# Performance work log

Measured on AMD Instinct MI355X. Metric: run time of the kernel, lower is better.

## Reference

```python
import jax, jax.numpy as jnp
import numpy as np

B, L, D = 16, 2048, 320          # batch, frames, mel_filter_size * mask_size (80*4)
CODE_DIM = 16                     # code_book_size (projection output dim)
NUM_CODES = 8192                  # num_code_books (codebook entries)
N_MASK = (B * L) // 2             # fixed number of masked positions (static for jit)


def setup_inputs() -> dict:
    key = jax.random.key(0)
    k1, k2, k3, k4 = jax.random.split(key, 4)
    input_values = jax.random.normal(k1, (B, L, D), dtype=jnp.float32)
    # mask with exactly N_MASK ones so the gather has a static size
    perm = jax.random.permutation(k2, B * L)
    mask_flat = jnp.zeros((B * L,), jnp.int32).at[perm[:N_MASK]].set(1)
    mask_time_indices = mask_flat.reshape(B, L)
    # xavier_uniform for Linear(D -> CODE_DIM), weight shape (CODE_DIM, D)
    limit = float(np.sqrt(6.0 / (D + CODE_DIM)))
    proj_weight = jax.random.uniform(k3, (CODE_DIM, D), jnp.float32, -limit, limit)
    code_book = jax.random.normal(k4, (NUM_CODES, CODE_DIM), dtype=jnp.float32)
    return {
        "input_values": input_values,
        "mask_time_indices": mask_time_indices,
        "proj_weight": proj_weight,
        "code_book": code_book,
    }


def reference(input_values, mask_time_indices, proj_weight, code_book):
    d = input_values.shape[-1]
    x = input_values.reshape(-1, d)                      # (B*L, D)
    mask = mask_time_indices.reshape(-1)
    idx = jnp.nonzero(mask == 1, size=N_MASK)[0]         # static-size gather of masked rows
    rows = x[idx]                                        # (N, D)
    targets = rows @ proj_weight.T                       # (N, CODE_DIM)
    # ||t - c||_2 via the GEMM expansion ||t||^2 + ||c||^2 - 2 t.c (avoids (N,K,S) blowup)
    t2 = jnp.sum(targets * targets, axis=-1, keepdims=True)       # (N, 1)
    c2 = jnp.sum(code_book * code_book, axis=-1)                  # (K,)
    d2 = t2 + c2[None, :] - 2.0 * (targets @ code_book.T)         # (N, K)
    dist = jnp.sqrt(jnp.maximum(d2, 0.0))
    # torch.argmin with no dim flattens -> scalar index into the (N*K) array
    labels = jnp.argmin(dist)
    return labels
```

## Files before the change

### kernel.cpp

```cpp
#include <hip/hip_runtime.h>
#include <hip/hip_bf16.h>


#define NMASK   16384
#define NROWS   32768
#define D       320
#define CDIM    16
#define NCODES  8192
#define EPS_C   0.0117f
#define EPS_ABS 0.02f

typedef __attribute__((ext_vector_type(8))) short short8;
typedef __attribute__((ext_vector_type(4))) float f32x4;

__device__ inline unsigned int encf(float f) {
  unsigned int u = __float_as_uint(f);
  return (u & 0x80000000u) ? ~u : (u | 0x80000000u);
}
__device__ inline float decf(unsigned int u) {
  unsigned int b = (u & 0x80000000u) ? (u & 0x7fffffffu) : ~u;
  return __uint_as_float(b);
}
__device__ inline unsigned short f2bf(float f) {
  unsigned int u = __float_as_uint(f);
  unsigned int r = u + 0x7fffu + ((u >> 16) & 1u);
  return (unsigned short)(r >> 16);
}
__device__ inline float bf2f(unsigned short h) {
  return __uint_as_float(((unsigned int)h) << 16);
}

__device__ inline void proj_lds(const float* __restrict__ x,
                                const float* __restrict__ Wl,
                                int row, int ch, float pd[16]) {
  const float* xr = x + (size_t)row * D + ch * 4;
  float4 xv[10];
#pragma unroll
  for (int j = 0; j < 10; ++j) xv[j] = *(const float4*)(xr + j * 32);
#pragma unroll
  for (int c = 0; c < 16; ++c) pd[c] = 0.f;
#pragma unroll
  for (int j = 0; j < 10; ++j) {
#pragma unroll
    for (int c = 0; c < 16; ++c) {
      const float4 wv = *(const float4*)&Wl[c * D + j * 32 + ch * 4];
      float acc = fmaf(xv[j].x, wv.x, pd[c]);
      acc = fmaf(xv[j].y, wv.y, acc);
      acc = fmaf(xv[j].z, wv.z, acc);
      pd[c] = fmaf(xv[j].w, wv.w, acc);
    }
  }
#pragma unroll
  for (int c = 0; c < 16; ++c) {
    pd[c] += __shfl_xor(pd[c], 1);
    pd[c] += __shfl_xor(pd[c], 2);
    pd[c] += __shfl_xor(pd[c], 4);
  }
}

__global__ void init_kernel(unsigned int* __restrict__ ctrs,
                            unsigned long long* __restrict__ key) {
  if (threadIdx.x < 4) ctrs[threadIdx.x] = 0u;
  if (threadIdx.x == 4) key[0] = 0xFFFFFFFFFFFFFFFFull;
}

__global__ __launch_bounds__(256) void project_kernel(
    const float* __restrict__ x, const int* __restrict__ mask,
    const float* __restrict__ W, const float* __restrict__ cbk,
    float* __restrict__ c2, unsigned short* __restrict__ cbf32,
    unsigned short* __restrict__ tbf32, float* __restrict__ t2arr,
    int* __restrict__ origrow, unsigned int* __restrict__ rowmin_u,
    unsigned int* __restrict__ slotctr) {
  __shared__ float Wl[CDIM * D];
  __shared__ unsigned long long mb;
  __shared__ unsigned int wcnt[4], wbase[4];
  int tid = threadIdx.x, bid = (int)blockIdx.x;
  int chunk = bid >> 1, half = bid & 1;
  for (int i = tid; i < (CDIM * D) / 4; i += 256)
    ((float4*)Wl)[i] = ((const float4*)W)[i];
  if (tid < 64) {
    int m = mask[chunk * 64 + tid];
    unsigned long long bal = __ballot(m != 0);
    if (tid == 0) mb = bal;
  }
  if (tid < 16) rowmin_u[bid * 16 + tid] = 0xFFFFFFFFu;
  __syncthreads();

  if (bid < 512 && tid < 16) {
    int k = bid * 16 + tid;
    const float4* p = (const float4*)(cbk + (long)k * CDIM);
    float s = 0.f; unsigned short nb[16];
#pragma unroll
    for (int q = 0; q < 4; ++q) {
      float4 v = p[q];
      s = fmaf(v.x, v.x, s); s = fmaf(v.y, v.y, s);
      s = fmaf(v.z, v.z, s); s = fmaf(v.w, v.w, s);
      nb[q*4+0] = f2bf(-2.0f * v.x); nb[q*4+1] = f2bf(-2.0f * v.y);
      nb[q*4+2] = f2bf(-2.0f * v.z); nb[q*4+3] = f2bf(-2.0f * v.w);
    }
    c2[k] = s;
    unsigned short g1 = f2bf(s);
    unsigned short g2 = f2bf(s - bf2f(g1));
    uint4 pk0, pk1, pk2, pk3;
    pk0.x = (unsigned int)nb[0]  | ((unsigned int)nb[1]  << 16);
    pk0.y = (unsigned int)nb[2]  | ((unsigned int)nb[3]  << 16);
    pk0.z = (unsigned int)nb[4]  | ((unsigned int)nb[5]  << 16);
    pk0.w = (unsigned int)nb[6]  | ((unsigned int)nb[7]  << 16);
    pk1.x = (unsigned int)nb[8]  | ((unsigned int)nb[9]  << 16);
    pk1.y = (unsigned int)nb[10] | ((unsigned int)nb[11] << 16);
    pk1.z = (unsigned int)nb[12] | ((unsigned int)nb[13] << 16);
    pk1.w = (unsigned int)nb[14] | ((unsigned int)nb[15] << 16);
    pk2.x = (unsigned int)g1 | ((unsigned int)g2 << 16);
    pk2.y = 0x3F803F80u;
    pk2.z = 0u; pk2.w = 0u;
    pk3.x = 0u; pk3.y = 0u; pk3.z = 0u; pk3.w = 0u;
    uint4* dst = (uint4*)(cbf32 + (long)k * 32);
    dst[0] = pk0; dst[1] = pk1; dst[2] = pk2; dst[3] = pk3;
  }

  unsigned long long B0 = mb;
  int r = tid >> 3, ch = tid & 7, lane = tid & 63, w = tid >> 6;
  int p = half * 32 + r;
  int row = chunk * 64 + p;
  int m = (int)((B0 >> p) & 1ull);

  unsigned long long wbal = __ballot(m && ch == 0);
  if (lane == 0) wcnt[w] = (unsigned int)__popcll(wbal);
  __syncthreads();
  if (tid == 0) {
    unsigned int tot = wcnt[0] + wcnt[1] + wcnt[2] + wcnt[3];
    unsigned int b = tot ? atomicAdd(slotctr, tot) : 0u;
    wbase[0] = b;
    wbase[1] = b + wcnt[0];
    wbase[2] = b + wcnt[0] + wcnt[1];
    wbase[3] = b + wcnt[0] + wcnt[1] + wcnt[2];
  }
  __syncthreads();
  if (!m) return;

  float pd[16];
  proj_lds(x, Wl, row, ch, pd);

  if (ch == 0) {
    int slot = (int)wbase[w] + __popcll(wbal & ((1ull << lane) - 1ull));
    float t2 = 0.f;
#pragma unroll
    for (int c = 0; c < 16; ++c) t2 = fmaf(pd[c], pd[c], t2);
    t2arr[slot] = t2;
    origrow[slot] = row;
    unsigned short tb[16];
#pragma unroll
    for (int c = 0; c < 16; ++c) tb[c] = f2bf(pd[c]);
    unsigned short h1 = f2bf(t2);
    unsigned short h2 = f2bf(t2 - bf2f(h1));
    uint4 pk0, pk1, pk2, pk3;
    pk0.x = (unsigned int)tb[0]  | ((unsigned int)tb[1]  << 16);
    pk0.y = (unsigned int)tb[2]  | ((unsigned int)tb[3]  << 16);
    pk0.z = (unsigned int)tb[4]  | ((unsigned int)tb[5]  << 16);
    pk0.w = (unsigned int)tb[6]  | ((unsigned int)tb[7]  << 16);
    pk1.x = (unsigned int)tb[8]  | ((unsigned int)tb[9]  << 16);
    pk1.y = (unsigned int)tb[10] | ((unsigned int)tb[11] << 16);
    pk1.z = (unsigned int)tb[12] | ((unsigned int)tb[13] << 16);
    pk1.w = (unsigned int)tb[14] | ((unsigned int)tb[15] << 16);
    pk2.x = 0x3F803F80u;
    pk2.y = (unsigned int)h1 | ((unsigned int)h2 << 16);
    pk2.z = 0u; pk2.w = 0u;
    pk3.x = 0u; pk3.y = 0u; pk3.z = 0u; pk3.w = 0u;
    uint4* dst = (uint4*)(tbf32 + (long)slot * 32);
    dst[0] = pk0; dst[1] = pk1; dst[2] = pk2; dst[3] = pk3;
  }
}

__global__ __launch_bounds__(256) void phase1_kernel(
    const unsigned short* __restrict__ tbf32,
    const unsigned short* __restrict__ cbf32,
    unsigned int* __restrict__ rowmin_u) {
  __shared__ unsigned int rml[4 * 33];
  int tid = threadIdx.x;
  int w = tid >> 6, l = tid & 63, lr = l & 15, g = l >> 4;
  int strip = (int)blockIdx.x >> 2;
  int seg   = ((int)blockIdx.x & 3) * 4 + w;
  int row0 = strip * 32;

  for (int i = tid; i < 4 * 33; i += 256) rml[i] = 0xFFFFFFFFu;
  __syncthreads();

  const f32x4 zero = {0.f, 0.f, 0.f, 0.f};
  short8 calA = {0,0,0,0,0,0,0,0}, calB = {0,0,0,0,0,0,0,0};
  if (g == 0) {
    calA[0] = (short)f2bf((float)(lr + 1));
    calB[0] = (short)0x3F80;
  }
  f32x4 cal = __builtin_amdgcn_mfma_f32_16x16x32_bf16(calA, calB, zero, 0, 0, 0);
  int rid[4];
#pragma unroll
  for (int j = 0; j < 4; ++j) {
    int v = (int)(cal[j] + 0.5f) - 1;
    rid[j] = v < 0 ? 0 : (v > 15 ? 15 : v);
  }

  const short8 a0 = *(const short8*)(tbf32 + (long)(row0 + lr) * 32 + g * 8);
  const short8 a1 = *(const short8*)(tbf32 + (long)(row0 + 16 + lr) * 32 + g * 8);
  f32x4 rmin0 = {3.4e38f, 3.4e38f, 3.4e38f, 3.4e38f};
  f32x4 rmin1 = rmin0;
  int code0 = seg * 512;
#pragma unroll 2
  for (int t = 0; t < 32; ++t) {
    int code = code0 + t * 16 + lr;
    short8 b = *(const short8*)(cbf32 + (long)code * 32 + g * 8);
    f32x4 d0 = __builtin_amdgcn_mfma_f32_16x16x32_bf16(a0, b, zero, 0, 0, 0);
    f32x4 d1 = __builtin_amdgcn_mfma_f32_16x16x32_bf16(a1, b, zero, 0, 0, 0);
#pragma unroll
    for (int j = 0; j < 4; ++j) {
      rmin0[j] = fminf(rmin0[j], d0[j]);
      rmin1[j] = fminf(rmin1[j], d1[j]);
    }
  }
  unsigned int* mywave = &rml[w * 33];
#pragma unroll
  for (int j = 0; j < 4; ++j) {
    atomicMin(&mywave[rid[j]],      encf(rmin0[j]));
    atomicMin(&mywave[16 + rid[j]], encf(rmin1[j]));
  }
  __syncthreads();
  if (tid < 32) {
    unsigned int mn = 0xFFFFFFFFu;
#pragma unroll
    for (int ww = 0; ww < 4; ++ww) mn = min(mn, rml[ww * 33 + tid]);
    atomicMin(&rowmin_u[row0 + tid], mn);
  }
}

__global__ __launch_bounds__(1024) void gate_kernel(
    const unsigned int* __restrict__ rowmin_u, const float* __restrict__ t2arr,
    const float* __restrict__ c2,
    unsigned int* __restrict__ candcount, int* __restrict__ candlist) {
  __shared__ float sT[1024];
  __shared__ float c2m_s;
  __shared__ unsigned int cnt;
  int tid = threadIdx.x;
  float cm = 0.f;
#pragma unroll
  for (int i = 0; i < 8; ++i) cm = fmaxf(cm, c2[tid + i * 1024]);
  sT[tid] = cm;
  if (tid == 0) cnt = 0u;
  __syncthreads();
  for (int st = 512; st > 0; st >>= 1) {
    if (tid < st) sT[tid] = fmaxf(sT[tid], sT[tid + st]);
    __syncthreads();
  }
  if (tid == 0) c2m_s = sT[0];
  __syncthreads();
  float c2m = c2m_s;
  float Tl = 3.4e38f;
  for (int i = tid; i < NMASK; i += 1024) {
    float a = decf(rowmin_u[i]);
    float e = fmaf(EPS_C, sqrtf(t2arr[i] * c2m), EPS_ABS);
    Tl = fminf(Tl, a + e);
  }
  sT[tid] = Tl;
  __syncthreads();
  for (int st = 512; st > 0; st >>= 1) {
    if (tid < st) sT[tid] = fminf(sT[tid], sT[tid + st]);
    __syncthreads();
  }
  float T = sT[0];
  for (int i = tid; i < NMASK; i += 1024) {
    float a = decf(rowmin_u[i]);
    float e = fmaf(EPS_C, sqrtf(t2arr[i] * c2m), EPS_ABS);
    if (!(a - e > T)) {
      unsigned int pos = atomicAdd(&cnt, 1u);
      candlist[pos] = i;
    }
  }
  __syncthreads();
  if (tid == 0) candcount[0] = cnt;
}

__global__ __launch_bounds__(256) void cproj_kernel(
    const float* __restrict__ x, const float* __restrict__ W,
    const int* __restrict__ origrow, const unsigned int* __restrict__ candcount,
    const int* __restrict__ candlist, float* __restrict__ tgtm) {
  int tid = threadIdx.x, bid = (int)blockIdx.x;
  int nc = (int)candcount[0];
  if (bid * 32 >= nc) return;
  __shared__ float Wl[CDIM * D];
  for (int i = tid; i < (CDIM * D) / 4; i += 256)
    ((float4*)Wl)[i] = ((const float4*)W)[i];
  __syncthreads();
  int idx = bid * 32 + (tid >> 3);
  int ch  = tid & 7;
  if (idx >= nc) return;
  int row = origrow[candlist[idx]];
  float pd[16];
  proj_lds(x, Wl, row, ch, pd);
  if (ch == 0) {
    float* op = tgtm + (long)idx * 16;
#pragma unroll
    for (int c = 0; c < 16; ++c) op[c] = -2.0f * pd[c];
  }
}

__global__ __launch_bounds__(256) void rescore_kernel(
    const float* __restrict__ cbk, const float* __restrict__ c2,
    const float* __restrict__ tgtm, const float* __restrict__ t2arr,
    const int* __restrict__ origrow, const int* __restrict__ mask,
    const unsigned int* __restrict__ candcount, const int* __restrict__ candlist,
    unsigned long long* __restrict__ key, unsigned int* __restrict__ resctr,
    int* __restrict__ out) {
  __shared__ unsigned long long red[256];
  __shared__ int lastf;
  __shared__ unsigned int vlow_s;
  int tid = threadIdx.x, bid = (int)blockIdx.x;
  int nwork = (int)candcount[0] * 8;
  for (int wk = bid; wk < nwork; wk += (int)gridDim.x) {
    int ci = wk >> 3, oct = wk & 7;
    int r = candlist[ci];
    float t2 = t2arr[r];
    int row = origrow[r];
    float tm[16];
    const float4* tp = (const float4*)(tgtm + (long)ci * 16);
#pragma unroll
    for (int q = 0; q < 4; ++q) {
      float4 v = tp[q];
      tm[q*4+0] = v.x; tm[q*4+1] = v.y; tm[q*4+2] = v.z; tm[q*4+3] = v.w;
    }
    float minv = 3.4e38f; int mink = 0;
#pragma unroll 2
    for (int k = 0; k < 4; ++k) {
      int code = oct * 1024 + k * 256 + tid;
      const float4* cp = (const float4*)(cbk + (long)code * CDIM);
      float4 c0 = cp[0], c1 = cp[1], c2v4 = cp[2], c3 = cp[3];
      float acc = fmaf(tm[0],  c0.x, c2[code]);
      acc = fmaf(tm[1],  c0.y, acc);   acc = fmaf(tm[2],  c0.z, acc);
      acc = fmaf(tm[3],  c0.w, acc);   acc = fmaf(tm[4],  c1.x, acc);
      acc = fmaf(tm[5],  c1.y, acc);   acc = fmaf(tm[6],  c1.z, acc);
      acc = fmaf(tm[7],  c1.w, acc);   acc = fmaf(tm[8],  c2v4.x, acc);
      acc = fmaf(tm[9],  c2v4.y, acc); acc = fmaf(tm[10], c2v4.z, acc);
      acc = fmaf(tm[11], c2v4.w, acc); acc = fmaf(tm[12], c3.x, acc);
      acc = fmaf(tm[13], c3.y, acc);   acc = fmaf(tm[14], c3.z, acc);
      acc = fmaf(tm[15], c3.w, acc);
      if (acc < minv) { minv = acc; mink = code; }
    }
    red[tid] = ((unsigned long long)encf(t2 + minv) << 32)
        | (unsigned long long)((unsigned int)row * (unsigned int)NCODES + (unsigned int)mink);
    __syncthreads();
    for (int s = 128; s > 0; s >>= 1) {
      if (tid < s) { if (red[tid + s] < red[tid]) red[tid] = red[tid + s]; }
      __syncthreads();
    }
    if (tid == 0) atomicMin(key, red[0]);
    __syncthreads();
  }
  if (tid == 0) {
    __threadfence();
    lastf = (atomicAdd(resctr, 1u) == (unsigned int)gridDim.x - 1u) ? 1 : 0;
  }
  __syncthreads();
  if (lastf) {
    if (tid == 0)
      vlow_s = (unsigned int)(atomicMin(key, 0xFFFFFFFFFFFFFFFFull) & 0xFFFFFFFFull);
    __syncthreads();
    unsigned int vlow = vlow_s;
    int wrow = (int)(vlow >> 13), wcode = (int)(vlow & 8191u);
    int lo = tid * (NROWS / 256);
    int hi = lo + (NROWS / 256); if (hi > wrow) hi = wrow;
    int cnt = 0;
#pragma unroll 4
    for (int i = lo; i < hi; ++i) cnt += (mask[i] != 0);
    __shared__ int ps[256];
    ps[tid] = cnt;
    __syncthreads();
    for (int s = 128; s > 0; s >>= 1) {
      if (tid < s) ps[tid] += ps[tid + s];
      __syncthreads();
    }
    if (tid == 0) out[0] = ps[0] * NCODES + wcode;
  }
}

extern "C" void kernel_launch(void* const* d_in, const int* in_sizes, int n_in,
                              void* d_out, int out_size, void* d_ws, size_t ws_size,
                              hipStream_t stream) {
  const float* x    = (const float*)d_in[0];
  const int*   mask = (const int*)d_in[1];
  const float* W    = (const float*)d_in[2];
  const float* cbk  = (const float*)d_in[3];
  int* out = (int*)d_out;

  char* ws = (char*)d_ws;
  unsigned int*       ctrs      = (unsigned int*)(ws + 4096);
  unsigned int*       resctr    = (unsigned int*)(ws + 4096);
  unsigned int*       slotctr   = (unsigned int*)(ws + 4100);
  unsigned int*       candcount = (unsigned int*)(ws + 4112);
  unsigned long long* key       = (unsigned long long*)(ws + 8184);
  unsigned int*       rowmin_u  = (unsigned int*)(ws + 8192);
  float*              t2arr     = (float*)(ws + 73728);
  int*                origrow   = (int*)(ws + 139264);
  float*              c2        = (float*)(ws + 204800);
  unsigned short*     cbf32     = (unsigned short*)(ws + 237568);
  int*                candlist  = (int*)(ws + 237568);
  unsigned short*     tbf32     = (unsigned short*)(ws + 761856);
  float*              tgtm      = (float*)(ws + 761856);

  init_kernel<<<1, 64, 0, stream>>>(ctrs, key);
  project_kernel<<<1024, 256, 0, stream>>>(x, mask, W, cbk, c2, cbf32, tbf32,
                                           t2arr, origrow, rowmin_u, slotctr);
  phase1_kernel<<<2048, 256, 0, stream>>>(tbf32, cbf32, rowmin_u);
  gate_kernel<<<1, 1024, 0, stream>>>(rowmin_u, t2arr, c2, candcount, candlist);
  cproj_kernel<<<512, 256, 0, stream>>>(x, W, origrow, candcount, candlist, tgtm);
  rescore_kernel<<<512, 256, 0, stream>>>(cbk, c2, tgtm, t2arr, origrow, mask,
                                          candcount, candlist, key, resctr, out);
}
```

Before: 89.37 us.

## Fuse gate, candidate projection and rescore into one single-block tail kernel

Merges the gate, candidate projection and rescore kernels into one 1024-thread single-block tail kernel, removing two launches, the global key atomics and the last-block counter. Phase1 now has each block cover all 8192 codes for its 32-row strip (512 blocks instead of 2048). Row minima can then be stored directly instead of reduced with atomicMin, so the rowmin init is dropped. The cost is that the whole rescore over candidates runs serially in one block, which becomes slow if many candidates pass the gate.

After: 124.6 us. +39.4%, slower.

```diff
diff --git a/kernel.cpp b/kernel.cpp
--- a/kernel.cpp
+++ b/kernel.cpp
@@ -58,10 +58,8 @@
   }
 }
 
-__global__ void init_kernel(unsigned int* __restrict__ ctrs,
-                            unsigned long long* __restrict__ key) {
+__global__ void init_kernel(unsigned int* __restrict__ ctrs) {
   if (threadIdx.x < 4) ctrs[threadIdx.x] = 0u;
-  if (threadIdx.x == 4) key[0] = 0xFFFFFFFFFFFFFFFFull;
 }
 
 __global__ __launch_bounds__(256) void project_kernel(
@@ -69,8 +67,7 @@
     const float* __restrict__ W, const float* __restrict__ cbk,
     float* __restrict__ c2, unsigned short* __restrict__ cbf32,
     unsigned short* __restrict__ tbf32, float* __restrict__ t2arr,
-    int* __restrict__ origrow, unsigned int* __restrict__ rowmin_u,
-    unsigned int* __restrict__ slotctr) {
+    int* __restrict__ origrow, unsigned int* __restrict__ slotctr) {
   __shared__ float Wl[CDIM * D];
   __shared__ unsigned long long mb;
   __shared__ unsigned int wcnt[4], wbase[4];
@@ -83,7 +80,6 @@
     unsigned long long bal = __ballot(m != 0);
     if (tid == 0) mb = bal;
   }
-  if (tid < 16) rowmin_u[bid * 16 + tid] = 0xFFFFFFFFu;
   __syncthreads();
 
   if (bid < 512 && tid < 16) {
@@ -178,12 +174,9 @@
   __shared__ unsigned int rml[4 * 33];
   int tid = threadIdx.x;
   int w = tid >> 6, l = tid & 63, lr = l & 15, g = l >> 4;
-  int strip = (int)blockIdx.x >> 2;
-  int seg   = ((int)blockIdx.x & 3) * 4 + w;
-  int row0 = strip * 32;
+  int row0 = (int)blockIdx.x * 32;
 
   for (int i = tid; i < 4 * 33; i += 256) rml[i] = 0xFFFFFFFFu;
-  __syncthreads();
 
   const f32x4 zero = {0.f, 0.f, 0.f, 0.f};
   short8 calA = {0,0,0,0,0,0,0,0}, calB = {0,0,0,0,0,0,0,0};
@@ -203,19 +196,23 @@
   const short8 a1 = *(const short8*)(tbf32 + (long)(row0 + 16 + lr) * 32 + g * 8);
   f32x4 rmin0 = {3.4e38f, 3.4e38f, 3.4e38f, 3.4e38f};
   f32x4 rmin1 = rmin0;
-  int code0 = seg * 512;
+#pragma unroll
+  for (int s4 = 0; s4 < 4; ++s4) {
+    int code0 = (s4 * 4 + w) * 512;
 #pragma unroll 2
-  for (int t = 0; t < 32; ++t) {
-    int code = code0 + t * 16 + lr;
-    short8 b = *(const short8*)(cbf32 + (long)code * 32 + g * 8);
-    f32x4 d0 = __builtin_amdgcn_mfma_f32_16x16x32_bf16(a0, b, zero, 0, 0, 0);
-    f32x4 d1 = __builtin_amdgcn_mfma_f32_16x16x32_bf16(a1, b, zero, 0, 0, 0);
-#pragma unroll
-    for (int j = 0; j < 4; ++j) {
-      rmin0[j] = fminf(rmin0[j], d0[j]);
-      rmin1[j] = fminf(rmin1[j], d1[j]);
-    }
-  }
+    for (int t = 0; t < 32; ++t) {
+      int code = code0 + t * 16 + lr;
+      short8 b = *(const short8*)(cbf32 + (long)code * 32 + g * 8);
+      f32x4 d0 = __builtin_amdgcn_mfma_f32_16x16x32_bf16(a0, b, zero, 0, 0, 0);
+      f32x4 d1 = __builtin_amdgcn_mfma_f32_16x16x32_bf16(a1, b, zero, 0, 0, 0);
+#pragma unroll
+      for (int j = 0; j < 4; ++j) {
+        rmin0[j] = fminf(rmin0[j], d0[j]);
+        rmin1[j] = fminf(rmin1[j], d1[j]);
+      }
+    }
+  }
+  __syncthreads();
   unsigned int* mywave = &rml[w * 33];
 #pragma unroll
   for (int j = 0; j < 4; ++j) {
@@ -227,97 +224,77 @@
     unsigned int mn = 0xFFFFFFFFu;
 #pragma unroll
     for (int ww = 0; ww < 4; ++ww) mn = min(mn, rml[ww * 33 + tid]);
-    atomicMin(&rowmin_u[row0 + tid], mn);
-  }
-}
-
-__global__ __launch_bounds__(1024) void gate_kernel(
-    const unsigned int* __restrict__ rowmin_u, const float* __restrict__ t2arr,
-    const float* __restrict__ c2,
-    unsigned int* __restrict__ candcount, int* __restrict__ candlist) {
-  __shared__ float sT[1024];
-  __shared__ float c2m_s;
-  __shared__ unsigned int cnt;
+    rowmin_u[row0 + tid] = mn;
+  }
+}
+
+__global__ __launch_bounds__(1024) void tail_kernel(
+    const float* __restrict__ x, const float* __restrict__ W,
+    const float* __restrict__ cbk, const float* __restrict__ c2,
+    const float* __restrict__ t2arr, const int* __restrict__ origrow,
+    const unsigned int* __restrict__ rowmin_u, const int* __restrict__ mask,
+    int* __restrict__ candlist, float* __restrict__ tgtm,
+    int* __restrict__ out) {
+  __shared__ float Wl[CDIM * D];
+  __shared__ float red_f[1024];
+  __shared__ unsigned long long red_u[1024];
+  __shared__ unsigned int cnt_s;
+  __shared__ unsigned int vlow_s;
   int tid = threadIdx.x;
+
+  for (int i = tid; i < (CDIM * D) / 4; i += 1024)
+    ((float4*)Wl)[i] = ((const float4*)W)[i];
   float cm = 0.f;
-#pragma unroll
-  for (int i = 0; i < 8; ++i) cm = fmaxf(cm, c2[tid + i * 1024]);
-  sT[tid] = cm;
-  if (tid == 0) cnt = 0u;
-  __syncthreads();
-  for (int st = 512; st > 0; st >>= 1) {
-    if (tid < st) sT[tid] = fmaxf(sT[tid], sT[tid + st]);
+  for (int i = tid; i < NCODES; i += 1024) cm = fmaxf(cm, c2[i]);
+  red_f[tid] = cm;
+  if (tid == 0) cnt_s = 0u;
+  __syncthreads();
+  for (int s = 512; s > 0; s >>= 1) {
+    if (tid < s) red_f[tid] = fmaxf(red_f[tid], red_f[tid + s]);
     __syncthreads();
   }
-  if (tid == 0) c2m_s = sT[0];
-  __syncthreads();
-  float c2m = c2m_s;
+  float c2m = red_f[0];
+  __syncthreads();
   float Tl = 3.4e38f;
   for (int i = tid; i < NMASK; i += 1024) {
     float a = decf(rowmin_u[i]);
     float e = fmaf(EPS_C, sqrtf(t2arr[i] * c2m), EPS_ABS);
     Tl = fminf(Tl, a + e);
   }
-  sT[tid] = Tl;
-  __syncthreads();
-  for (int st = 512; st > 0; st >>= 1) {
-    if (tid < st) sT[tid] = fminf(sT[tid], sT[tid + st]);
+  red_f[tid] = Tl;
+  __syncthreads();
+  for (int s = 512; s > 0; s >>= 1) {
+    if (tid < s) red_f[tid] = fminf(red_f[tid], red_f[tid + s]);
     __syncthreads();
   }
-  float T = sT[0];
+  float T = red_f[0];
   for (int i = tid; i < NMASK; i += 1024) {
     float a = decf(rowmin_u[i]);
     float e = fmaf(EPS_C, sqrtf(t2arr[i] * c2m), EPS_ABS);
     if (!(a - e > T)) {
-      unsigned int pos = atomicAdd(&cnt, 1u);
+      unsigned int pos = atomicAdd(&cnt_s, 1u);
       candlist[pos] = i;
     }
   }
   __syncthreads();
-  if (tid == 0) candcount[0] = cnt;
-}
-
-__global__ __launch_bounds__(256) void cproj_kernel(
-    const float* __restrict__ x, const float* __restrict__ W,
-    const int* __restrict__ origrow, const unsigned int* __restrict__ candcount,
-    const int* __restrict__ candlist, float* __restrict__ tgtm) {
-  int tid = threadIdx.x, bid = (int)blockIdx.x;
-  int nc = (int)candcount[0];
-  if (bid * 32 >= nc) return;
-  __shared__ float Wl[CDIM * D];
-  for (int i = tid; i < (CDIM * D) / 4; i += 256)
-    ((float4*)Wl)[i] = ((const float4*)W)[i];
-  __syncthreads();
-  int idx = bid * 32 + (tid >> 3);
-  int ch  = tid & 7;
-  if (idx >= nc) return;
-  int row = origrow[candlist[idx]];
-  float pd[16];
-  proj_lds(x, Wl, row, ch, pd);
-  if (ch == 0) {
-    float* op = tgtm + (long)idx * 16;
-#pragma unroll
-    for (int c = 0; c < 16; ++c) op[c] = -2.0f * pd[c];
-  }
-}
-
-__global__ __launch_bounds__(256) void rescore_kernel(
-    const float* __restrict__ cbk, const float* __restrict__ c2,
-    const float* __restrict__ tgtm, const float* __restrict__ t2arr,
-    const int* __restrict__ origrow, const int* __restrict__ mask,
-    const unsigned int* __restrict__ candcount, const int* __restrict__ candlist,
-    unsigned long long* __restrict__ key, unsigned int* __restrict__ resctr,
-    int* __restrict__ out) {
-  __shared__ unsigned long long red[256];
-  __shared__ int lastf;
-  __shared__ unsigned int vlow_s;
-  int tid = threadIdx.x, bid = (int)blockIdx.x;
-  int nwork = (int)candcount[0] * 8;
-  for (int wk = bid; wk < nwork; wk += (int)gridDim.x) {
-    int ci = wk >> 3, oct = wk & 7;
-    int r = candlist[ci];
-    float t2 = t2arr[r];
-    int row = origrow[r];
+  int nc = (int)cnt_s;
+  int grp = tid >> 3, ch = tid & 7;
+  for (int idx = grp; idx < nc; idx += 128) {
+    int row = origrow[candlist[idx]];
+    float pd[16];
+    proj_lds(x, Wl, row, ch, pd);
+    if (ch == 0) {
+      float* op = tgtm + (long)idx * 16;
+#pragma unroll
+      for (int c = 0; c < 16; ++c) op[c] = -2.0f * pd[c];
+    }
+  }
+  __syncthreads();
+  unsigned long long best = 0xFFFFFFFFFFFFFFFFull;
+  for (int ci = 0; ci < nc; ++ci) {
+    int slot = candlist[ci];
+    float t2 = t2arr[slot];
+    int row = origrow[slot];
     float tm[16];
     const float4* tp = (const float4*)(tgtm + (long)ci * 16);
 #pragma unroll
@@ -325,10 +302,9 @@
       float4 v = tp[q];
       tm[q*4+0] = v.x; tm[q*4+1] = v.y; tm[q*4+2] = v.z; tm[q*4+3] = v.w;
     }
-    float minv = 3.4e38f; int mink = 0;
 #pragma unroll 2
-    for (int k = 0; k < 4; ++k) {
-      int code = oct * 1024 + k * 256 + tid;
+    for (int k = 0; k < 8; ++k) {
+      int code = k * 1024 + tid;
       const float4* cp = (const float4*)(cbk + (long)code * CDIM);
       float4 c0 = cp[0], c1 = cp[1], c2v4 = cp[2], c3 = cp[3];
       float acc = fmaf(tm[0],  c0.x, c2[code]);
@@ -340,43 +316,34 @@
       acc = fmaf(tm[11], c2v4.w, acc); acc = fmaf(tm[12], c3.x, acc);
       acc = fmaf(tm[13], c3.y, acc);   acc = fmaf(tm[14], c3.z, acc);
       acc = fmaf(tm[15], c3.w, acc);
-      if (acc < minv) { minv = acc; mink = code; }
-    }
-    red[tid] = ((unsigned long long)encf(t2 + minv) << 32)
-        | (unsigned long long)((unsigned int)row * (unsigned int)NCODES + (unsigned int)mink);
+      unsigned long long pk = ((unsigned long long)encf(t2 + acc) << 32)
+          | (unsigned long long)((unsigned int)row * (unsigned int)NCODES
+                                 + (unsigned int)code);
+      best = (pk < best) ? pk : best;
+    }
+  }
+  red_u[tid] = best;
+  __syncthreads();
+  for (int s = 512; s > 0; s >>= 1) {
+    if (tid < s) { if (red_u[tid + s] < red_u[tid]) red_u[tid] = red_u[tid + s]; }
     __syncthreads();
-    for (int s = 128; s > 0; s >>= 1) {
-      if (tid < s) { if (red[tid + s] < red[tid]) red[tid] = red[tid + s]; }
-      __syncthreads();
-    }
-    if (tid == 0) atomicMin(key, red[0]);
+  }
+  if (tid == 0) vlow_s = (unsigned int)(red_u[0] & 0xFFFFFFFFull);
+  __syncthreads();
+  unsigned int vlow = vlow_s;
+  int wrow = (int)(vlow >> 13), wcode = (int)(vlow & 8191u);
+  int lo = tid * (NROWS / 1024);
+  int hi = lo + (NROWS / 1024); if (hi > wrow) hi = wrow;
+  int cnt = 0;
+#pragma unroll 4
+  for (int i = lo; i < hi; ++i) cnt += (mask[i] != 0);
+  red_u[tid] = (unsigned long long)cnt;
+  __syncthreads();
+  for (int s = 512; s > 0; s >>= 1) {
+    if (tid < s) red_u[tid] += red_u[tid + s];
     __syncthreads();
   }
-  if (tid == 0) {
-    __threadfence();
-    lastf = (atomicAdd(resctr, 1u) == (unsigned int)gridDim.x - 1u) ? 1 : 0;
-  }
-  __syncthreads();
-  if (lastf) {
-    if (tid == 0)
-      vlow_s = (unsigned int)(atomicMin(key, 0xFFFFFFFFFFFFFFFFull) & 0xFFFFFFFFull);
-    __syncthreads();
-    unsigned int vlow = vlow_s;
-    int wrow = (int)(vlow >> 13), wcode = (int)(vlow & 8191u);
-    int lo = tid * (NROWS / 256);
-    int hi = lo + (NROWS / 256); if (hi > wrow) hi = wrow;
-    int cnt = 0;
-#pragma unroll 4
-    for (int i = lo; i < hi; ++i) cnt += (mask[i] != 0);
-    __shared__ int ps[256];
-    ps[tid] = cnt;
-    __syncthreads();
-    for (int s = 128; s > 0; s >>= 1) {
-      if (tid < s) ps[tid] += ps[tid + s];
-      __syncthreads();
-    }
-    if (tid == 0) out[0] = ps[0] * NCODES + wcode;
-  }
+  if (tid == 0) out[0] = (int)red_u[0] * NCODES + wcode;
 }
 
 extern "C" void kernel_launch(void* const* d_in, const int* in_sizes, int n_in,
@@ -390,10 +357,7 @@
 
   char* ws = (char*)d_ws;
   unsigned int*       ctrs      = (unsigned int*)(ws + 4096);
-  unsigned int*       resctr    = (unsigned int*)(ws + 4096);
-  unsigned int*       slotctr   = (unsigned int*)(ws + 4100);
-  unsigned int*       candcount = (unsigned int*)(ws + 4112);
-  unsigned long long* key       = (unsigned long long*)(ws + 8184);
+  unsigned int*       slotctr   = (unsigned int*)(ws + 4096);
   unsigned int*       rowmin_u  = (unsigned int*)(ws + 8192);
   float*              t2arr     = (float*)(ws + 73728);
   int*                origrow   = (int*)(ws + 139264);
@@ -403,12 +367,10 @@
   unsigned short*     tbf32     = (unsigned short*)(ws + 761856);
   float*              tgtm      = (float*)(ws + 761856);
 
-  init_kernel<<<1, 64, 0, stream>>>(ctrs, key);
+  init_kernel<<<1, 64, 0, stream>>>(ctrs);
   project_kernel<<<1024, 256, 0, stream>>>(x, mask, W, cbk, c2, cbf32, tbf32,
-                                           t2arr, origrow, rowmin_u, slotctr);
-  phase1_kernel<<<2048, 256, 0, stream>>>(tbf32, cbf32, rowmin_u);
-  gate_kernel<<<1, 1024, 0, stream>>>(rowmin_u, t2arr, c2, candcount, candlist);
-  cproj_kernel<<<512, 256, 0, stream>>>(x, W, origrow, candcount, candlist, tgtm);
-  rescore_kernel<<<512, 256, 0, stream>>>(cbk, c2, tgtm, t2arr, origrow, mask,
-                                          candcount, candlist, key, resctr, out);
-}
+                                           t2arr, origrow, slotctr);
+  phase1_kernel<<<512, 256, 0, stream>>>(tbf32, cbf32, rowmin_u);
+  tail_kernel<<<1, 1024, 0, stream>>>(x, W, cbk, c2, t2arr, origrow, rowmin_u,
+                                      mask, candlist, tgtm, out);
+}
```

## Make phase1 own full codebook per strip and fuse gate with candidate projection

Applied to the files above, without the earlier changes.

Each phase1 block now loops over all 16 codebook segments for its 32-row strip, so it writes row minima directly instead of doing global atomicMin, and project_kernel no longer has to initialize rowmin_u. The gate kernel and candidate projection kernel are merged into one single-block kernel, which removes a launch and the candcount readback. In exchange, phase1 launches 4x fewer blocks with 4x longer loops, and candidate projection now runs on only one workgroup, so it is serialized if many candidates pass the gate.

Result: slower. 115.7 us (+29.5%).

```diff
diff --git a/kernel.cpp b/kernel.cpp
--- a/kernel.cpp
+++ b/kernel.cpp
@@ -69,8 +69,7 @@
     const float* __restrict__ W, const float* __restrict__ cbk,
     float* __restrict__ c2, unsigned short* __restrict__ cbf32,
     unsigned short* __restrict__ tbf32, float* __restrict__ t2arr,
-    int* __restrict__ origrow, unsigned int* __restrict__ rowmin_u,
-    unsigned int* __restrict__ slotctr) {
+    int* __restrict__ origrow, unsigned int* __restrict__ slotctr) {
   __shared__ float Wl[CDIM * D];
   __shared__ unsigned long long mb;
   __shared__ unsigned int wcnt[4], wbase[4];
@@ -83,7 +82,6 @@
     unsigned long long bal = __ballot(m != 0);
     if (tid == 0) mb = bal;
   }
-  if (tid < 16) rowmin_u[bid * 16 + tid] = 0xFFFFFFFFu;
   __syncthreads();
 
   if (bid < 512 && tid < 16) {
@@ -178,12 +176,9 @@
   __shared__ unsigned int rml[4 * 33];
   int tid = threadIdx.x;
   int w = tid >> 6, l = tid & 63, lr = l & 15, g = l >> 4;
-  int strip = (int)blockIdx.x >> 2;
-  int seg   = ((int)blockIdx.x & 3) * 4 + w;
-  int row0 = strip * 32;
+  int row0 = (int)blockIdx.x * 32;
 
   for (int i = tid; i < 4 * 33; i += 256) rml[i] = 0xFFFFFFFFu;
-  __syncthreads();
 
   const f32x4 zero = {0.f, 0.f, 0.f, 0.f};
   short8 calA = {0,0,0,0,0,0,0,0}, calB = {0,0,0,0,0,0,0,0};
@@ -203,19 +198,23 @@
   const short8 a1 = *(const short8*)(tbf32 + (long)(row0 + 16 + lr) * 32 + g * 8);
   f32x4 rmin0 = {3.4e38f, 3.4e38f, 3.4e38f, 3.4e38f};
   f32x4 rmin1 = rmin0;
-  int code0 = seg * 512;
+#pragma unroll
+  for (int s4 = 0; s4 < 4; ++s4) {
+    int code0 = (s4 * 4 + w) * 512;
 #pragma unroll 2
-  for (int t = 0; t < 32; ++t) {
-    int code = code0 + t * 16 + lr;
-    short8 b = *(const short8*)(cbf32 + (long)code * 32 + g * 8);
-    f32x4 d0 = __builtin_amdgcn_mfma_f32_16x16x32_bf16(a0, b, zero, 0, 0, 0);
-    f32x4 d1 = __builtin_amdgcn_mfma_f32_16x16x32_bf16(a1, b, zero, 0, 0, 0);
-#pragma unroll
-    for (int j = 0; j < 4; ++j) {
-      rmin0[j] = fminf(rmin0[j], d0[j]);
-      rmin1[j] = fminf(rmin1[j], d1[j]);
-    }
-  }
+    for (int t = 0; t < 32; ++t) {
+      int code = code0 + t * 16 + lr;
+      short8 b = *(const short8*)(cbf32 + (long)code * 32 + g * 8);
+      f32x4 d0 = __builtin_amdgcn_mfma_f32_16x16x32_bf16(a0, b, zero, 0, 0, 0);
+      f32x4 d1 = __builtin_amdgcn_mfma_f32_16x16x32_bf16(a1, b, zero, 0, 0, 0);
+#pragma unroll
+      for (int j = 0; j < 4; ++j) {
+        rmin0[j] = fminf(rmin0[j], d0[j]);
+        rmin1[j] = fminf(rmin1[j], d1[j]);
+      }
+    }
+  }
+  __syncthreads();
   unsigned int* mywave = &rml[w * 33];
 #pragma unroll
   for (int j = 0; j < 4; ++j) {
@@ -227,77 +226,68 @@
     unsigned int mn = 0xFFFFFFFFu;
 #pragma unroll
     for (int ww = 0; ww < 4; ++ww) mn = min(mn, rml[ww * 33 + tid]);
-    atomicMin(&rowmin_u[row0 + tid], mn);
-  }
-}
-
-__global__ __launch_bounds__(1024) void gate_kernel(
-    const unsigned int* __restrict__ rowmin_u, const float* __restrict__ t2arr,
-    const float* __restrict__ c2,
-    unsigned int* __restrict__ candcount, int* __restrict__ candlist) {
-  __shared__ float sT[1024];
-  __shared__ float c2m_s;
-  __shared__ unsigned int cnt;
+    rowmin_u[row0 + tid] = mn;
+  }
+}
+
+__global__ __launch_bounds__(1024) void gatecp_kernel(
+    const float* __restrict__ x, const float* __restrict__ W,
+    const float* __restrict__ c2, const float* __restrict__ t2arr,
+    const int* __restrict__ origrow, const unsigned int* __restrict__ rowmin_u,
+    unsigned int* __restrict__ candcount, int* __restrict__ candlist,
+    float* __restrict__ tgtm) {
+  __shared__ float Wl[CDIM * D];
+  __shared__ float red_f[1024];
+  __shared__ unsigned int cnt_s;
   int tid = threadIdx.x;
+
+  for (int i = tid; i < (CDIM * D) / 4; i += 1024)
+    ((float4*)Wl)[i] = ((const float4*)W)[i];
   float cm = 0.f;
-#pragma unroll
-  for (int i = 0; i < 8; ++i) cm = fmaxf(cm, c2[tid + i * 1024]);
-  sT[tid] = cm;
-  if (tid == 0) cnt = 0u;
-  __syncthreads();
-  for (int st = 512; st > 0; st >>= 1) {
-    if (tid < st) sT[tid] = fmaxf(sT[tid], sT[tid + st]);
-    __syncthreads();
-  }
-  if (tid == 0) c2m_s = sT[0];
-  __syncthreads();
-  float c2m = c2m_s;
+  for (int i = tid; i < NCODES; i += 1024) cm = fmaxf(cm, c2[i]);
+  red_f[tid] = cm;
+  if (tid == 0) cnt_s = 0u;
+  __syncthreads();
+  for (int s = 512; s > 0; s >>= 1) {
+    if (tid < s) red_f[tid] = fmaxf(red_f[tid], red_f[tid + s]);
+    __syncthreads();
+  }
+  float c2m = red_f[0];
+  __syncthreads();
   float Tl = 3.4e38f;
   for (int i = tid; i < NMASK; i += 1024) {
     float a = decf(rowmin_u[i]);
     float e = fmaf(EPS_C, sqrtf(t2arr[i] * c2m), EPS_ABS);
     Tl = fminf(Tl, a + e);
   }
-  sT[tid] = Tl;
-  __syncthreads();
-  for (int st = 512; st > 0; st >>= 1) {
-    if (tid < st) sT[tid] = fminf(sT[tid], sT[tid + st]);
-    __syncthreads();
-  }
-  float T = sT[0];
+  red_f[tid] = Tl;
+  __syncthreads();
+  for (int s = 512; s > 0; s >>= 1) {
+    if (tid < s) red_f[tid] = fminf(red_f[tid], red_f[tid + s]);
+    __syncthreads();
+  }
+  float T = red_f[0];
   for (int i = tid; i < NMASK; i += 1024) {
     float a = decf(rowmin_u[i]);
     float e = fmaf(EPS_C, sqrtf(t2arr[i] * c2m), EPS_ABS);
     if (!(a - e > T)) {
-      unsigned int pos = atomicAdd(&cnt, 1u);
+      unsigned int pos = atomicAdd(&cnt_s, 1u);
       candlist[pos] = i;
     }
   }
   __syncthreads();
-  if (tid == 0) candcount[0] = cnt;
-}
-
-__global__ __launch_bounds__(256) void cproj_kernel(
-    const float* __restrict__ x, const float* __restrict__ W,
-    const int* __restrict__ origrow, const unsigned int* __restrict__ candcount,
-    const int* __restrict__ candlist, float* __restrict__ tgtm) {
-  int tid = threadIdx.x, bid = (int)blockIdx.x;
-  int nc = (int)candcount[0];
-  if (bid * 32 >= nc) return;
-  __shared__ float Wl[CDIM * D];
-  for (int i = tid; i < (CDIM * D) / 4; i += 256)
-    ((float4*)Wl)[i] = ((const float4*)W)[i];
-  __syncthreads();
-  int idx = bid * 32 + (tid >> 3);
-  int ch  = tid & 7;
-  if (idx >= nc) return;
-  int row = origrow[candlist[idx]];
-  float pd[16];
-  proj_lds(x, Wl, row, ch, pd);
-  if (ch == 0) {
-    float* op = tgtm + (long)idx * 16;
-#pragma unroll
-    for (int c = 0; c < 16; ++c) op[c] = -2.0f * pd[c];
+  int nc = (int)cnt_s;
+  if (tid == 0) candcount[0] = cnt_s;
+  int grp = tid >> 3, ch = tid & 7;
+  for (int idx = grp; idx < nc; idx += 128) {
+    int row = origrow[candlist[idx]];
+    float pd[16];
+    proj_lds(x, Wl, row, ch, pd);
+    if (ch == 0) {
+      float* op = tgtm + (long)idx * 16;
+#pragma unroll
+      for (int c = 0; c < 16; ++c) op[c] = -2.0f * pd[c];
+    }
   }
 }
 
@@ -390,8 +380,8 @@
 
   char* ws = (char*)d_ws;
   unsigned int*       ctrs      = (unsigned int*)(ws + 4096);
-  unsigned int*       resctr    = (unsigned int*)(ws + 4096);
-  unsigned int*       slotctr   = (unsigned int*)(ws + 4100);
+  unsigned int*       slotctr   = (unsigned int*)(ws + 4096);
+  unsigned int*       resctr    = (unsigned int*)(ws + 4100);
   unsigned int*       candcount = (unsigned int*)(ws + 4112);
   unsigned long long* key       = (unsigned long long*)(ws + 8184);
   unsigned int*       rowmin_u  = (unsigned int*)(ws + 8192);
@@ -405,10 +395,10 @@
 
   init_kernel<<<1, 64, 0, stream>>>(ctrs, key);
   project_kernel<<<1024, 256, 0, stream>>>(x, mask, W, cbk, c2, cbf32, tbf32,
-                                           t2arr, origrow, rowmin_u, slotctr);
-  phase1_kernel<<<2048, 256, 0, stream>>>(tbf32, cbf32, rowmin_u);
-  gate_kernel<<<1, 1024, 0, stream>>>(rowmin_u, t2arr, c2, candcount, candlist);
-  cproj_kernel<<<512, 256, 0, stream>>>(x, W, origrow, candcount, candlist, tgtm);
+                                           t2arr, origrow, slotctr);
+  phase1_kernel<<<512, 256, 0, stream>>>(tbf32, cbf32, rowmin_u);
+  gatecp_kernel<<<1, 1024, 0, stream>>>(x, W, c2, t2arr, origrow, rowmin_u,
+                                        candcount, candlist, tgtm);
   rescore_kernel<<<512, 256, 0, stream>>>(cbk, c2, tgtm, t2arr, origrow, mask,
                                           candcount, candlist, key, resctr, out);
 }
```

## Compact masked rows per block and project two rows per thread group

Applied to the files above, without the earlier changes.

The projection kernel now handles 128 rows per block instead of 32. It first builds a compacted list of the masked rows in shared memory, so every thread group does useful work rather than idling on unmasked rows. Each 8-lane group computes two masked rows at once and reuses every W load from LDS for both, and the grid shrinks from 1024 to 256 blocks, which cuts redundant W staging to LDS. In exchange there are fewer blocks to fill the GPU, higher register pressure from the dual accumulators, and a small slot-counter/resctr offset swap.

After: 96.93 us. 1.08x slower.

```diff
diff --git a/kernel.cpp b/kernel.cpp
--- a/kernel.cpp
+++ b/kernel.cpp
@@ -56,6 +56,37 @@
     pd[c] += __shfl_xor(pd[c], 2);
     pd[c] += __shfl_xor(pd[c], 4);
   }
+}
+
+__device__ inline void store_t(const float pd[16], int slot, int row,
+                               float* __restrict__ t2arr,
+                               int* __restrict__ origrow,
+                               unsigned short* __restrict__ tbf32) {
+  float t2 = 0.f;
+#pragma unroll
+  for (int c = 0; c < 16; ++c) t2 = fmaf(pd[c], pd[c], t2);
+  t2arr[slot] = t2;
+  origrow[slot] = row;
+  unsigned short tb[16];
+#pragma unroll
+  for (int c = 0; c < 16; ++c) tb[c] = f2bf(pd[c]);
+  unsigned short h1 = f2bf(t2);
+  unsigned short h2 = f2bf(t2 - bf2f(h1));
+  uint4 pk0, pk1, pk2, pk3;
+  pk0.x = (unsigned int)tb[0]  | ((unsigned int)tb[1]  << 16);
+  pk0.y = (unsigned int)tb[2]  | ((unsigned int)tb[3]  << 16);
+  pk0.z = (unsigned int)tb[4]  | ((unsigned int)tb[5]  << 16);
+  pk0.w = (unsigned int)tb[6]  | ((unsigned int)tb[7]  << 16);
+  pk1.x = (unsigned int)tb[8]  | ((unsigned int)tb[9]  << 16);
+  pk1.y = (unsigned int)tb[10] | ((unsigned int)tb[11] << 16);
+  pk1.z = (unsigned int)tb[12] | ((unsigned int)tb[13] << 16);
+  pk1.w = (unsigned int)tb[14] | ((unsigned int)tb[15] << 16);
+  pk2.x = 0x3F803F80u;
+  pk2.y = (unsigned int)h1 | ((unsigned int)h2 << 16);
+  pk2.z = 0u; pk2.w = 0u;
+  pk3.x = 0u; pk3.y = 0u; pk3.z = 0u; pk3.w = 0u;
+  uint4* dst = (uint4*)(tbf32 + (long)slot * 32);
+  dst[0] = pk0; dst[1] = pk1; dst[2] = pk2; dst[3] = pk3;
 }
 
 __global__ void init_kernel(unsigned int* __restrict__ ctrs,
@@ -72,22 +103,23 @@
     int* __restrict__ origrow, unsigned int* __restrict__ rowmin_u,
     unsigned int* __restrict__ slotctr) {
   __shared__ float Wl[CDIM * D];
-  __shared__ unsigned long long mb;
-  __shared__ unsigned int wcnt[4], wbase[4];
+  __shared__ unsigned long long mbs[2];
+  __shared__ int pos[128];
+  __shared__ unsigned int base_s;
   int tid = threadIdx.x, bid = (int)blockIdx.x;
-  int chunk = bid >> 1, half = bid & 1;
+  int rbase = bid * 128;
   for (int i = tid; i < (CDIM * D) / 4; i += 256)
     ((float4*)Wl)[i] = ((const float4*)W)[i];
-  if (tid < 64) {
-    int m = mask[chunk * 64 + tid];
+  if (tid < 128) {
+    int m = mask[rbase + tid];
     unsigned long long bal = __ballot(m != 0);
-    if (tid == 0) mb = bal;
-  }
-  if (tid < 16) rowmin_u[bid * 16 + tid] = 0xFFFFFFFFu;
-  __syncthreads();
-
-  if (bid < 512 && tid < 16) {
-    int k = bid * 16 + tid;
+    if ((tid & 63) == 0) mbs[tid >> 6] = bal;
+  }
+  if (tid < 64) rowmin_u[bid * 64 + tid] = 0xFFFFFFFFu;
+  __syncthreads();
+
+  if (tid < 32) {
+    int k = bid * 32 + tid;
     const float4* p = (const float4*)(cbk + (long)k * CDIM);
     float s = 0.f; unsigned short nb[16];
 #pragma unroll
@@ -118,56 +150,72 @@
     dst[0] = pk0; dst[1] = pk1; dst[2] = pk2; dst[3] = pk3;
   }
 
-  unsigned long long B0 = mb;
-  int r = tid >> 3, ch = tid & 7, lane = tid & 63, w = tid >> 6;
-  int p = half * 32 + r;
-  int row = chunk * 64 + p;
-  int m = (int)((B0 >> p) & 1ull);
-
-  unsigned long long wbal = __ballot(m && ch == 0);
-  if (lane == 0) wcnt[w] = (unsigned int)__popcll(wbal);
-  __syncthreads();
-  if (tid == 0) {
-    unsigned int tot = wcnt[0] + wcnt[1] + wcnt[2] + wcnt[3];
-    unsigned int b = tot ? atomicAdd(slotctr, tot) : 0u;
-    wbase[0] = b;
-    wbase[1] = b + wcnt[0];
-    wbase[2] = b + wcnt[0] + wcnt[1];
-    wbase[3] = b + wcnt[0] + wcnt[1] + wcnt[2];
-  }
-  __syncthreads();
-  if (!m) return;
-
-  float pd[16];
-  proj_lds(x, Wl, row, ch, pd);
-
-  if (ch == 0) {
-    int slot = (int)wbase[w] + __popcll(wbal & ((1ull << lane) - 1ull));
-    float t2 = 0.f;
-#pragma unroll
-    for (int c = 0; c < 16; ++c) t2 = fmaf(pd[c], pd[c], t2);
-    t2arr[slot] = t2;
-    origrow[slot] = row;
-    unsigned short tb[16];
-#pragma unroll
-    for (int c = 0; c < 16; ++c) tb[c] = f2bf(pd[c]);
-    unsigned short h1 = f2bf(t2);
-    unsigned short h2 = f2bf(t2 - bf2f(h1));
-    uint4 pk0, pk1, pk2, pk3;
-    pk0.x = (unsigned int)tb[0]  | ((unsigned int)tb[1]  << 16);
-    pk0.y = (unsigned int)tb[2]  | ((unsigned int)tb[3]  << 16);
-    pk0.z = (unsigned int)tb[4]  | ((unsigned int)tb[5]  << 16);
-    pk0.w = (unsigned int)tb[6]  | ((unsigned int)tb[7]  << 16);
-    pk1.x = (unsigned int)tb[8]  | ((unsigned int)tb[9]  << 16);
-    pk1.y = (unsigned int)tb[10] | ((unsigned int)tb[11] << 16);
-    pk1.z = (unsigned int)tb[12] | ((unsigned int)tb[13] << 16);
-    pk1.w = (unsigned int)tb[14] | ((unsigned int)tb[15] << 16);
-    pk2.x = 0x3F803F80u;
-    pk2.y = (unsigned int)h1 | ((unsigned int)h2 << 16);
-    pk2.z = 0u; pk2.w = 0u;
-    pk3.x = 0u; pk3.y = 0u; pk3.z = 0u; pk3.w = 0u;
-    uint4* dst = (uint4*)(tbf32 + (long)slot * 32);
-    dst[0] = pk0; dst[1] = pk1; dst[2] = pk2; dst[3] = pk3;
+  unsigned long long B0 = mbs[0], B1 = mbs[1];
+  int cnt0 = __popcll(B0);
+  int cnt  = cnt0 + __popcll(B1);
+  if (tid < 64 && ((B0 >> tid) & 1ull))
+    pos[__popcll(B0 & ((1ull << tid) - 1ull))] = tid;
+  if (tid >= 64 && tid < 128 && ((B1 >> (tid - 64)) & 1ull))
+    pos[cnt0 + __popcll(B1 & ((1ull << (tid - 64)) - 1ull))] = tid;
+  if (tid == 0) base_s = cnt ? atomicAdd(slotctr, (unsigned int)cnt) : 0u;
+  __syncthreads();
+  unsigned int base = base_s;
+
+  int r = tid >> 3, ch = tid & 7;
+  int idx0 = r, idx1 = r + 32;
+  if (idx1 < cnt) {
+    int row0 = rbase + pos[idx0], row1 = rbase + pos[idx1];
+    const float* xr0 = x + (size_t)row0 * D + ch * 4;
+    const float* xr1 = x + (size_t)row1 * D + ch * 4;
+    float4 xv0[10], xv1[10];
+#pragma unroll
+    for (int j = 0; j < 10; ++j) { xv0[j] = *(const float4*)(xr0 + j * 32);
+                                   xv1[j] = *(const float4*)(xr1 + j * 32); }
+    float pd0[16], pd1[16];
+#pragma unroll
+    for (int c = 0; c < 16; ++c) { pd0[c] = 0.f; pd1[c] = 0.f; }
+#pragma unroll
+    for (int j = 0; j < 10; ++j) {
+#pragma unroll
+      for (int c = 0; c < 16; ++c) {
+        const float4 wv = *(const float4*)&Wl[c * D + j * 32 + ch * 4];
+        float a0 = fmaf(xv0[j].x, wv.x, pd0[c]);
+        a0 = fmaf(xv0[j].y, wv.y, a0);
+        a0 = fmaf(xv0[j].z, wv.z, a0);
+        pd0[c] = fmaf(xv0[j].w, wv.w, a0);
+        float a1 = fmaf(xv1[j].x, wv.x, pd1[c]);
+        a1 = fmaf(xv1[j].y, wv.y, a1);
+        a1 = fmaf(xv1[j].z, wv.z, a1);
+        pd1[c] = fmaf(xv1[j].w, wv.w, a1);
+      }
+    }
+#pragma unroll
+    for (int c = 0; c < 16; ++c) {
+      pd0[c] += __shfl_xor(pd0[c], 1);
+      pd0[c] += __shfl_xor(pd0[c], 2);
+      pd0[c] += __shfl_xor(pd0[c], 4);
+    }
+#pragma unroll
+    for (int c = 0; c < 16; ++c) {
+      pd1[c] += __shfl_xor(pd1[c], 1);
+      pd1[c] += __shfl_xor(pd1[c], 2);
+      pd1[c] += __shfl_xor(pd1[c], 4);
+    }
+    if (ch == 0) {
+      store_t(pd0, (int)base + idx0, row0, t2arr, origrow, tbf32);
+      store_t(pd1, (int)base + idx1, row1, t2arr, origrow, tbf32);
+    }
+  } else if (idx0 < cnt) {
+    int row = rbase + pos[idx0];
+    float pd[16];
+    proj_lds(x, Wl, row, ch, pd);
+    if (ch == 0) store_t(pd, (int)base + idx0, row, t2arr, origrow, tbf32);
+  }
+  for (int idx = r + 64; idx < cnt; idx += 32) {
+    int row = rbase + pos[idx];
+    float pd[16];
+    proj_lds(x, Wl, row, ch, pd);
+    if (ch == 0) store_t(pd, (int)base + idx, row, t2arr, origrow, tbf32);
   }
 }
 
@@ -235,21 +283,21 @@
     const unsigned int* __restrict__ rowmin_u, const float* __restrict__ t2arr,
     const float* __restrict__ c2,
     unsigned int* __restrict__ candcount, int* __restrict__ candlist) {
-  __shared__ float sT[1024];
+  __shared__ float red_f[1024];
   __shared__ float c2m_s;
   __shared__ unsigned int cnt;
   int tid = threadIdx.x;
   float cm = 0.f;
 #pragma unroll
   for (int i = 0; i < 8; ++i) cm = fmaxf(cm, c2[tid + i * 1024]);
-  sT[tid] = cm;
+  red_f[tid] = cm;
   if (tid == 0) cnt = 0u;
   __syncthreads();
   for (int st = 512; st > 0; st >>= 1) {
-    if (tid < st) sT[tid] = fmaxf(sT[tid], sT[tid + st]);
-    __syncthreads();
-  }
-  if (tid == 0) c2m_s = sT[0];
+    if (tid < st) red_f[tid] = fmaxf(red_f[tid], red_f[tid + st]);
+    __syncthreads();
+  }
+  if (tid == 0) c2m_s = red_f[0];
   __syncthreads();
   float c2m = c2m_s;
   float Tl = 3.4e38f;
@@ -258,13 +306,13 @@
     float e = fmaf(EPS_C, sqrtf(t2arr[i] * c2m), EPS_ABS);
     Tl = fminf(Tl, a + e);
   }
-  sT[tid] = Tl;
+  red_f[tid] = Tl;
   __syncthreads();
   for (int st = 512; st > 0; st >>= 1) {
-    if (tid < st) sT[tid] = fminf(sT[tid], sT[tid + st]);
-    __syncthreads();
-  }
-  float T = sT[0];
+    if (tid < st) red_f[tid] = fminf(red_f[tid], red_f[tid + st]);
+    __syncthreads();
+  }
+  float T = red_f[0];
   for (int i = tid; i < NMASK; i += 1024) {
     float a = decf(rowmin_u[i]);
     float e = fmaf(EPS_C, sqrtf(t2arr[i] * c2m), EPS_ABS);
@@ -390,8 +438,8 @@
 
   char* ws = (char*)d_ws;
   unsigned int*       ctrs      = (unsigned int*)(ws + 4096);
-  unsigned int*       resctr    = (unsigned int*)(ws + 4096);
-  unsigned int*       slotctr   = (unsigned int*)(ws + 4100);
+  unsigned int*       slotctr   = (unsigned int*)(ws + 4096);
+  unsigned int*       resctr    = (unsigned int*)(ws + 4100);
   unsigned int*       candcount = (unsigned int*)(ws + 4112);
   unsigned long long* key       = (unsigned long long*)(ws + 8184);
   unsigned int*       rowmin_u  = (unsigned int*)(ws + 8192);
@@ -404,8 +452,8 @@
   float*              tgtm      = (float*)(ws + 761856);
 
   init_kernel<<<1, 64, 0, stream>>>(ctrs, key);
-  project_kernel<<<1024, 256, 0, stream>>>(x, mask, W, cbk, c2, cbf32, tbf32,
-                                           t2arr, origrow, rowmin_u, slotctr);
+  project_kernel<<<256, 256, 0, stream>>>(x, mask, W, cbk, c2, cbf32, tbf32,
+                                          t2arr, origrow, rowmin_u, slotctr);
   phase1_kernel<<<2048, 256, 0, stream>>>(tbf32, cbf32, rowmin_u);
   gate_kernel<<<1, 1024, 0, stream>>>(rowmin_u, t2arr, c2, candcount, candlist);
   cproj_kernel<<<512, 256, 0, stream>>>(x, W, origrow, candcount, candlist, tgtm);
```
